# Kernel tuning notes

Measured on AMD Instinct MI355X. Metric: run time of the kernel, lower is better.

Reference implementation:

```python
import jax, jax.numpy as jnp
import numpy as np
from jax import lax

B, L, C_IN, D, H = 256, 4096, 2, 128, 4
DH = D // H          # 32 head dim
FF = 192             # round_up(1.3 * 128, 64)
NUM_CLASSES = 5
EPS = 1e-5


def setup_inputs() -> dict:
    key = jax.random.key(0)
    it = iter(jax.random.split(key, 48))
    def r(*s):
        return jax.random.normal(next(it), s, jnp.float32) * 0.1
    return dict(
        x=jax.random.normal(next(it), (B, L, C_IN), jnp.float32),
        w1a=r(16, C_IN, 4), w1b=r(16, C_IN, 2),
        bn1_g=jnp.ones((32,), jnp.float32), bn1_b=jnp.zeros((32,), jnp.float32),
        bn1_m=r(32), bn1_v=jnp.ones((32,), jnp.float32),
        w2=r(64, 32, 3),
        bn2_g=jnp.ones((64,), jnp.float32), bn2_b=jnp.zeros((64,), jnp.float32),
        bn2_m=r(64), bn2_v=jnp.ones((64,), jnp.float32),
        w3=r(D, 64, 3),
        bn3_g=jnp.ones((D,), jnp.float32), bn3_b=jnp.zeros((D,), jnp.float32),
        bn3_m=r(D), bn3_v=jnp.ones((D,), jnp.float32),
        ln1_w=jnp.ones((D,), jnp.float32),
        conv_w=r(D, 1, 3), conv_b=jnp.zeros((D,), jnp.float32),
        wi=r(H, DH, DH), wf=r(H, DH, DH), wz=r(H, DH, DH), wo=r(H, DH, DH),
        rkernel=r(H, DH, 4, DH), rbias=r(4, H, DH),
        gn_w=jnp.ones((D,), jnp.float32),
        ln2_w=jnp.ones((D,), jnp.float32),
        ffn_up_w=r(D, 2 * FF), ffn_down_w=r(FF, D),
        lnp_w=jnp.ones((D,), jnp.float32),
        fc_w=r(D, NUM_CLASSES), fc_b=jnp.zeros((NUM_CLASSES,), jnp.float32),
        lengths=jnp.full((B,), L, jnp.int32),
    )


def _leaky(x):
    return jnp.where(x >= 0, x, 0.01 * x)


def _bn(x, g, b, m, v):  # eval-mode batchnorm, x: (B, C, L)
    return (x - m[:, None]) * (g / jnp.sqrt(v + EPS))[:, None] + b[:, None]


def _conv(x, w, pad, groups=1):  # x: (B, C, L), w: (O, I/groups, K)
    return lax.conv_general_dilated(x, w, (1,), [pad],
                                    dimension_numbers=('NCH', 'OIH', 'NCH'),
                                    feature_group_count=groups)


def _pool(x):  # max pool kernel=2 stride=2 (floor)
    b, c, l = x.shape
    l2 = l // 2
    return x[:, :, :l2 * 2].reshape(b, c, l2, 2).max(-1)


def _ln(x, w):  # LayerNorm, weight only (xlstm lib default bias=False)
    mu = jnp.mean(x, -1, keepdims=True)
    var = jnp.mean((x - mu) ** 2, -1, keepdims=True)
    return (x - mu) * lax.rsqrt(var + EPS) * w


def _forward(x, w1a, w1b, bn1_g, bn1_b, bn1_m, bn1_v, w2, bn2_g, bn2_b, bn2_m, bn2_v,
             w3, bn3_g, bn3_b, bn3_m, bn3_v, ln1_w, conv_w, conv_b, wi, wf, wz, wo,
             rkernel, rbias, gn_w, ln2_w, ffn_up_w, ffn_down_w, lnp_w, fc_w, fc_b, lengths):
    b = x.shape[0]
    # ---- CNN stem (dropout = identity in eval) ----
    xc = jnp.transpose(x, (0, 2, 1))                      # (B, C_in, L)
    h = jnp.concatenate([_conv(xc, w1a, (1, 1)), _conv(xc, w1b, (0, 0))], 1)  # (B, 32, L-1)
    h = _pool(_leaky(_bn(h, bn1_g, bn1_b, bn1_m, bn1_v)))
    h = _pool(_leaky(_bn(_conv(h, w2, (0, 0)), bn2_g, bn2_b, bn2_m, bn2_v)))
    h = _pool(_leaky(_bn(_conv(h, w3, (0, 0)), bn3_g, bn3_b, bn3_m, bn3_v)))
    e = jnp.transpose(h, (0, 2, 1))                       # (B, S, D)
    s = e.shape[1]

    # ---- sLSTM block: pre-LN -> sLSTM layer -> residual ----
    xn = _ln(e, ln1_w)
    # causal depthwise conv (k=3, left pad 2) + SiLU, feeds i/f gates
    xcv = _conv(jnp.transpose(xn, (0, 2, 1)), conv_w, (2, 0), groups=D)
    xcv = jnp.transpose(jax.nn.silu(xcv + conv_b[:, None]), (0, 2, 1))  # (B, S, D)

    def hproj(t, w):  # headwise (block-diagonal) linear
        return jnp.einsum('bshd,hde->bshe', t.reshape(b, s, H, DH), w)

    gx = jnp.stack([hproj(xcv, wi), hproj(xcv, wf), hproj(xn, wz), hproj(xn, wo)], 2)
    gx = jnp.transpose(gx, (1, 0, 2, 3, 4)) + rbias       # (S, B, 4, H, DH)

    def step(carry, g):
        y, c, n, m = carry                                # each (B, H, DH)
        raw = g + jnp.einsum('bhd,hdge->bghe', y, rkernel)  # (B, 4, H, DH)
        iraw, fraw, zraw, oraw = raw[:, 0], raw[:, 1], raw[:, 2], raw[:, 3]
        logfplusm = m + jax.nn.log_sigmoid(fraw)
        mnew = jnp.maximum(iraw, logfplusm)               # stabilizer
        ig = jnp.exp(iraw - mnew)
        fg = jnp.exp(logfplusm - mnew)
        cnew = fg * c + ig * jnp.tanh(zraw)
        nnew = fg * n + ig
        ynew = jax.nn.sigmoid(oraw) * cnew / nnew
        return (ynew, cnew, nnew, mnew), ynew

    z0 = jnp.zeros((b, H, DH), e.dtype)
    _, ys = lax.scan(step, (z0, z0, z0, z0), gx)          # ys: (S, B, H, DH)
    y = jnp.transpose(ys, (1, 0, 2, 3))                   # (B, S, H, DH)
    mu = jnp.mean(y, -1, keepdims=True)
    var = jnp.mean((y - mu) ** 2, -1, keepdims=True)
    y = ((y - mu) * lax.rsqrt(var + EPS)).reshape(b, s, D) * gn_w  # per-head groupnorm
    e = e + y

    # ---- gated GELU feedforward -> residual ----
    xn2 = _ln(e, ln2_w)
    up = xn2 @ ffn_up_w                                   # (B, S, 2*FF)
    e = e + (jax.nn.gelu(up[..., :FF], approximate=False) * up[..., FF:]) @ ffn_down_w

    # ---- post-stack norm, last token, classifier head ----
    e = _ln(e, lnp_w)
    return e[:, -1, :] @ fc_w + fc_b                      # (B, NUM_CLASSES)


def reference(x, w1a, w1b, bn1_g, bn1_b, bn1_m, bn1_v, w2, bn2_g, bn2_b, bn2_m, bn2_v,
              w3, bn3_g, bn3_b, bn3_m, bn3_v, ln1_w, conv_w, conv_b, wi, wf, wz, wo,
              rkernel, rbias, gn_w, ln2_w, ffn_up_w, ffn_down_w, lnp_w, fc_w, fc_b, lengths):
    return _forward(x, w1a, w1b, bn1_g, bn1_b, bn1_m, bn1_v, w2, bn2_g, bn2_b, bn2_m, bn2_v,
                    w3, bn3_g, bn3_b, bn3_m, bn3_v, ln1_w, conv_w, conv_b, wi, wf, wz, wo,
                    rkernel, rbias, gn_w, ln2_w, ffn_up_w, ffn_down_w, lnp_w, fc_w, fc_b, lengths)
```

## Files before the change

kernel.cpp:

```cpp
#include <hip/hip_runtime.h>
#include <hip/hip_bf16.h>
#include <math.h>

#define EPS 1e-5f

typedef __attribute__((ext_vector_type(8))) _Float16 half8;
typedef __attribute__((ext_vector_type(4))) float f32x4;

static __device__ __forceinline__ unsigned short f16u(float x) {
  _Float16 h = (_Float16)x;
  return *(unsigned short*)&h;
}
static __device__ __forceinline__ float uf16(unsigned short u) {
  _Float16 h = *(_Float16*)&u;
  return (float)h;
}

__global__ __launch_bounds__(256) void kWTB2(const float* __restrict__ w2,
    const float* __restrict__ w3, unsigned short* __restrict__ o2,
    unsigned short* __restrict__ o3) {
  int idx = blockIdx.x * 256 + threadIdx.x;
  if (idx < 64 * 104) {
    int oc = idx / 104, kp = idx % 104;
    float v = 0.f;
    if (kp < 96) { int k = kp >> 5, ci = kp & 31; v = w2[oc * 96 + ci * 3 + k]; }
    o2[idx] = f16u(v);
  } else {
    int j = idx - 64 * 104;
    if (j < 128 * 200) {
      int oc = j / 200, kp = j % 200;
      float v = 0.f;
      if (kp < 192) { int k = kp >> 6, ci = kp & 63; v = w3[oc * 192 + ci * 3 + k]; }
      o3[j] = f16u(v);
    }
  }
}

__global__ __launch_bounds__(512) void kConv12(const float* __restrict__ x,
    const float* __restrict__ w1a, const float* __restrict__ w1b,
    const float* __restrict__ g1, const float* __restrict__ b1,
    const float* __restrict__ m1, const float* __restrict__ v1,
    const unsigned short* __restrict__ Bw, const float* __restrict__ g2,
    const float* __restrict__ b2, const float* __restrict__ m2,
    const float* __restrict__ v2, unsigned short* __restrict__ out2) {
  __shared__ _Float16 sA[130 * 40];
  __shared__ _Float16 sB[64 * 104];
  int tid = threadIdx.x;
  int b = blockIdx.z;
  int p0 = blockIdx.x * 128;
  {
    const unsigned int* src = (const unsigned int*)Bw;
    unsigned int* dst = (unsigned int*)sB;
    for (int i = tid; i < 64 * 104 / 2; i += 512) dst[i] = src[i];
  }
  {
    int c = tid & 31, rg = tid >> 5;
    float sc1 = g1[c] * rsqrtf(v1[c] + EPS);
    float sh1 = b1[c] - m1[c] * sc1;
    float wk0[4], wk1[4];
    if (c < 16) {
#pragma unroll
      for (int k = 0; k < 4; k++) { wk0[k] = w1a[c * 8 + k]; wk1[k] = w1a[c * 8 + 4 + k]; }
    } else {
      int cc = c - 16;
#pragma unroll
      for (int k = 0; k < 2; k++) { wk0[k] = w1b[cc * 4 + k]; wk1[k] = w1b[cc * 4 + 2 + k]; }
      wk0[2] = wk0[3] = wk1[2] = wk1[3] = 0.f;
    }
    const float2* xp = (const float2*)(x + (size_t)b * 8192);
    for (int r = rg; r < 130; r += 16) {
      int rr = p0 + r;
      _Float16 outv = (_Float16)0.f;
      if (rr < 2047) {
        float xv0[5], xv1[5];
#pragma unroll
        for (int j = 0; j < 5; j++) {
          int l = 2 * rr - 1 + j;
          if (l >= 0 && l < 4096) { float2 v = xp[l]; xv0[j] = v.x; xv1[j] = v.y; }
          else { xv0[j] = 0.f; xv1[j] = 0.f; }
        }
        float a0 = 0.f, a1 = 0.f;
        if (c < 16) {
#pragma unroll
          for (int k = 0; k < 4; k++) {
            a0 += xv0[k] * wk0[k] + xv1[k] * wk1[k];
            a1 += xv0[k + 1] * wk0[k] + xv1[k + 1] * wk1[k];
          }
        } else {
#pragma unroll
          for (int k = 0; k < 2; k++) {
            a0 += xv0[k + 1] * wk0[k] + xv1[k + 1] * wk1[k];
            a1 += xv0[k + 2] * wk0[k] + xv1[k + 2] * wk1[k];
          }
        }
        a0 = a0 * sc1 + sh1; a1 = a1 * sc1 + sh1;
        a0 = a0 >= 0.f ? a0 : 0.01f * a0;
        a1 = a1 >= 0.f ? a1 : 0.01f * a1;
        outv = (_Float16)fmaxf(a0, a1);
      }
      sA[r * 40 + c] = outv;
    }
  }
  __syncthreads();
  int lane = tid & 63, w = tid >> 6;
  int nrow = lane & 15, quad = lane >> 4;
  f32x4 acc[4];
#pragma unroll
  for (int i = 0; i < 4; i++) acc[i] = (f32x4){0.f, 0.f, 0.f, 0.f};
  int mbase = w * 16;
#pragma unroll
  for (int kk = 0; kk < 3; kk++) {
    half8 a = *(const half8*)(sA + (mbase + nrow + kk) * 40 + quad * 8);
#pragma unroll
    for (int ot = 0; ot < 4; ot++) {
      half8 bb = *(const half8*)(sB + (ot * 16 + nrow) * 104 + kk * 32 + quad * 8);
      acc[ot] = __builtin_amdgcn_mfma_f32_16x16x32_f16(a, bb, acc[ot], 0, 0, 0);
    }
  }
  int gm0 = p0 + mbase + quad * 4;
#pragma unroll
  for (int ot = 0; ot < 4; ot++) {
    int oc = ot * 16 + nrow;
    float sc = g2[oc] * rsqrtf(v2[oc] + EPS);
    float sh = b2[oc] - m2[oc] * sc;
    float v0 = acc[ot][0] * sc + sh, vv1 = acc[ot][1] * sc + sh;
    float v2e = acc[ot][2] * sc + sh, v3 = acc[ot][3] * sc + sh;
    v0 = v0 >= 0.f ? v0 : 0.01f * v0;
    vv1 = vv1 >= 0.f ? vv1 : 0.01f * vv1;
    v2e = v2e >= 0.f ? v2e : 0.01f * v2e;
    v3 = v3 >= 0.f ? v3 : 0.01f * v3;
    float pA = fmaxf(v0, vv1), pB = fmaxf(v2e, v3);
    int t0 = gm0 >> 1, t1 = t0 + 1;
    if (t0 < 1022) out2[((size_t)b * 1022 + t0) * 64 + oc] = f16u(pA);
    if (t1 < 1022) out2[((size_t)b * 1022 + t1) * 64 + oc] = f16u(pB);
  }
}

__global__ __launch_bounds__(512) void kConv3LN(const unsigned short* __restrict__ in,
    const unsigned short* __restrict__ Bw, const float* __restrict__ g,
    const float* __restrict__ bta, const float* __restrict__ mn,
    const float* __restrict__ vr, const float* __restrict__ lnw,
    unsigned short* __restrict__ xn, float* __restrict__ elast) {
  constexpr int IC = 64, OC = 128, LIN = 1022, AP = 72, BP = 200, KSTEPS = 6, OCT = 8;
  __shared__ _Float16 sA[130 * AP];
  __shared__ _Float16 sB[OC * BP];
  int tid = threadIdx.x;
  int b = blockIdx.z;
  int p0 = blockIdx.x * 128;
  {
    const unsigned int* src = (const unsigned int*)Bw;
    unsigned int* dst = (unsigned int*)sB;
    for (int i = tid; i < OC * BP / 2; i += 512) dst[i] = src[i];
  }
  {
    int q = tid % 8;
    for (int r = tid / 8; r < 130; r += 64) {
      int gp = p0 + r;
      uint4 val = {0u, 0u, 0u, 0u};
      if (gp < LIN) val = *(const uint4*)(in + ((size_t)b * LIN + gp) * IC + q * 8);
      *(uint4*)(sA + r * AP + q * 8) = val;
    }
  }
  __syncthreads();
  int lane = tid & 63, w = tid >> 6;
  int nrow = lane & 15, quad = lane >> 4;
  f32x4 acc[OCT];
#pragma unroll
  for (int i = 0; i < OCT; i++) acc[i] = (f32x4){0.f, 0.f, 0.f, 0.f};
  int mbase = w * 16;
#pragma unroll
  for (int kk = 0; kk < KSTEPS; kk++) {
    int k = kk >> 1;
    int ci0 = (kk & 1) * 32;
    half8 a = *(const half8*)(sA + (mbase + nrow + k) * AP + ci0 + quad * 8);
#pragma unroll
    for (int ot = 0; ot < OCT; ot++) {
      half8 bb = *(const half8*)(sB + (ot * 16 + nrow) * BP + kk * 32 + quad * 8);
      acc[ot] = __builtin_amdgcn_mfma_f32_16x16x32_f16(a, bb, acc[ot], 0, 0, 0);
    }
  }
  float pA[OCT], pB[OCT];
  float sA1 = 0.f, sA2 = 0.f, sB1 = 0.f, sB2 = 0.f;
#pragma unroll
  for (int ot = 0; ot < OCT; ot++) {
    int oc = ot * 16 + nrow;
    float sc = g[oc] * rsqrtf(vr[oc] + EPS);
    float sh = bta[oc] - mn[oc] * sc;
    float v0 = acc[ot][0] * sc + sh, v1 = acc[ot][1] * sc + sh;
    float v2 = acc[ot][2] * sc + sh, v3 = acc[ot][3] * sc + sh;
    v0 = v0 >= 0.f ? v0 : 0.01f * v0;
    v1 = v1 >= 0.f ? v1 : 0.01f * v1;
    v2 = v2 >= 0.f ? v2 : 0.01f * v2;
    v3 = v3 >= 0.f ? v3 : 0.01f * v3;
    float a = fmaxf(v0, v1), bb2 = fmaxf(v2, v3);
    pA[ot] = a; pB[ot] = bb2;
    sA1 += a; sA2 += a * a; sB1 += bb2; sB2 += bb2 * bb2;
  }
#pragma unroll
  for (int m = 1; m <= 8; m <<= 1) {
    sA1 += __shfl_xor(sA1, m); sA2 += __shfl_xor(sA2, m);
    sB1 += __shfl_xor(sB1, m); sB2 += __shfl_xor(sB2, m);
  }
  float muA = sA1 * (1.f / 128.f);
  float rsA = rsqrtf(sA2 * (1.f / 128.f) - muA * muA + EPS);
  float muB = sB1 * (1.f / 128.f);
  float rsB = rsqrtf(sB2 * (1.f / 128.f) - muB * muB + EPS);
  int t0 = (p0 + mbase + quad * 4) >> 1, t1 = t0 + 1;
#pragma unroll
  for (int ot = 0; ot < OCT; ot++) {
    int oc = ot * 16 + nrow;
    float lw = lnw[oc];
    if (t0 < 510) xn[((size_t)b * 510 + t0) * OC + oc] = f16u((pA[ot] - muA) * rsA * lw);
    if (t1 < 510) xn[((size_t)b * 510 + t1) * OC + oc] = f16u((pB[ot] - muB) * rsB * lw);
    if (t1 == 509) elast[b * 128 + oc] = pB[ot];
  }
}

__global__ __launch_bounds__(256) void kGxM(const unsigned short* __restrict__ xn,
    const float* __restrict__ cw, const float* __restrict__ cb,
    const float* __restrict__ wi, const float* __restrict__ wf,
    const float* __restrict__ wz, const float* __restrict__ wo,
    const float* __restrict__ rb, unsigned int* __restrict__ gx) {
  __shared__ __align__(16) char smem[29200];
  float* xnf = (float*)smem;
  _Float16* aX = (_Float16*)(smem + 8720);
  _Float16* aN = (_Float16*)(smem + 13840);
  unsigned short* ct = (unsigned short*)smem;
  _Float16* sW = (_Float16*)(smem + 18960);
  int bh = blockIdx.x, b = bh >> 2, h = bh & 3;
  int tid = threadIdx.x, lane = tid & 63, w = tid >> 6;
  int nrow = lane & 15, quad = lane >> 4;
  for (int idx = tid; idx < 4096; idx += 256) {
    int slot = idx >> 11, n = (idx >> 5) & 63, d = idx & 31;
    const float* wp = slot ? ((n >= 32) ? wo : wz) : ((n >= 32) ? wf : wi);
    sW[slot * 2560 + n * 40 + d] = (_Float16)wp[h * 1024 + d * 32 + (n & 31)];
  }
  int dd = tid & 31;
  float cw0 = cw[(h * 32 + dd) * 3], cw1 = cw[(h * 32 + dd) * 3 + 1],
        cw2 = cw[(h * 32 + dd) * 3 + 2], cbv = cb[h * 32 + dd];
  float bias0[4], bias1[4];
#pragma unroll
  for (int nt = 0; nt < 4; nt++) {
    int n = nt * 16 + nrow;
    bias0[nt] = rb[(n >> 5) * 128 + h * 32 + (n & 31)];
    bias1[nt] = rb[(2 + (n >> 5)) * 128 + h * 32 + (n & 31)];
  }
  __syncthreads();
  half8 bw0[4], bw1[4];
#pragma unroll
  for (int nt = 0; nt < 4; nt++) {
    bw0[nt] = *(const half8*)(sW + (nt * 16 + nrow) * 40 + quad * 8);
    bw1[nt] = *(const half8*)(sW + 2560 + (nt * 16 + nrow) * 40 + quad * 8);
  }
  const unsigned short* xb = xn + ((size_t)b * 510) * 128 + h * 32;
  for (int s0 = 0; s0 < 510; s0 += 64) {
    __syncthreads();
    {
      int d2 = tid & 15;
      for (int r = tid >> 4; r < 66; r += 16) {
        int s = s0 - 2 + r;
        unsigned int v = 0;
        if (s >= 0 && s < 510) v = *(const unsigned int*)(xb + (size_t)s * 128 + d2 * 2);
        xnf[r * 33 + d2 * 2]     = uf16(v & 0xFFFFu);
        xnf[r * 33 + d2 * 2 + 1] = uf16(v >> 16);
      }
    }
    __syncthreads();
    for (int m = tid >> 5; m < 64; m += 8) {
      float x0 = xnf[m * 33 + dd], x1 = xnf[(m + 1) * 33 + dd], x2 = xnf[(m + 2) * 33 + dd];
      float a = cbv + cw0 * x0 + cw1 * x1 + cw2 * x2;
      a = a * __builtin_amdgcn_rcpf(1.f + __expf(-a));
      aX[m * 40 + dd] = (_Float16)a;
      aN[m * 40 + dd] = (_Float16)x2;
    }
    __syncthreads();
    f32x4 z = (f32x4){0.f, 0.f, 0.f, 0.f};
    half8 ax = *(const half8*)(aX + (w * 16 + nrow) * 40 + quad * 8);
    half8 an = *(const half8*)(aN + (w * 16 + nrow) * 40 + quad * 8);
    f32x4 acc0[4], acc1[4];
#pragma unroll
    for (int nt = 0; nt < 4; nt++) {
      acc0[nt] = __builtin_amdgcn_mfma_f32_16x16x32_f16(ax, bw0[nt], z, 0, 0, 0);
      acc1[nt] = __builtin_amdgcn_mfma_f32_16x16x32_f16(an, bw1[nt], z, 0, 0, 0);
    }
    __syncthreads();
#pragma unroll
    for (int nt = 0; nt < 4; nt++) {
#pragma unroll
      for (int r = 0; r < 4; r++) {
        int row = w * 16 + quad * 4 + r;
        ct[row * 132 + 2 * (nt * 16 + nrow)]     = f16u(acc0[nt][r] + bias0[nt]);
        ct[row * 132 + 2 * (nt * 16 + nrow) + 1] = f16u(acc1[nt][r] + bias1[nt]);
      }
    }
    __syncthreads();
    {
      int u = tid & 63;
      for (int m = tid >> 6; m < 64; m += 4) {
        int s = s0 + m;
        if (s < 510)
          gx[((size_t)s * 1024 + bh) * 64 + u] = *(const unsigned int*)(ct + m * 132 + 2 * u);
      }
    }
  }
}

__global__ __launch_bounds__(64) void kRec(const unsigned int* __restrict__ gx,
    const float* __restrict__ rk, float* __restrict__ yf) {
  int bh = blockIdx.x; int h = bh & 3;
  int l = threadIdx.x; int half = l >> 5; int e = l & 31;
  float R1[32], R2[32];
  int g1 = half, g2 = 2 + half;
  const float* r1p = rk + h * 4096 + g1 * 32 + e;
  const float* r2p = rk + h * 4096 + g2 * 32 + e;
#pragma unroll
  for (int d = 0; d < 32; d++) { R1[d] = r1p[d * 128]; R2[d] = r2p[d * 128]; }
  const unsigned int* gp = gx + (size_t)bh * 64 + l;
  unsigned int p0 = gp[0], p1 = gp[65536], p2 = gp[131072], p3 = gp[196608];
  float y = 0.f, cst = 0.f, nst = 0.f, mst = 0.f;
  for (int s = 0; s < 510; s++) {
    unsigned int pc = p0; p0 = p1; p1 = p2; p2 = p3;
    if (s + 4 < 510) p3 = gp[(size_t)(s + 4) * 65536];
    float a1 = uf16(pc & 0xFFFFu);
    float a2 = uf16(pc >> 16);
    float s10 = 0.f, s11 = 0.f, s12 = 0.f, s13 = 0.f;
    float s20 = 0.f, s21 = 0.f, s22 = 0.f, s23 = 0.f;
    unsigned int yb = __float_as_uint(y);
#pragma unroll
    for (int d = 0; d < 32; d += 4) {
      float y0 = __uint_as_float(__builtin_amdgcn_readlane(yb, d));
      float y1 = __uint_as_float(__builtin_amdgcn_readlane(yb, d + 1));
      float y2 = __uint_as_float(__builtin_amdgcn_readlane(yb, d + 2));
      float y3 = __uint_as_float(__builtin_amdgcn_readlane(yb, d + 3));
      s10 = fmaf(y0, R1[d], s10);     s20 = fmaf(y0, R2[d], s20);
      s11 = fmaf(y1, R1[d + 1], s11); s21 = fmaf(y1, R2[d + 1], s21);
      s12 = fmaf(y2, R1[d + 2], s12); s22 = fmaf(y2, R2[d + 2], s22);
      s13 = fmaf(y3, R1[d + 3], s13); s23 = fmaf(y3, R2[d + 3], s23);
    }
    a1 += (s10 + s11) + (s12 + s13);
    a2 += (s20 + s21) + (s22 + s23);
    float en = __expf(-fabsf(a1));
    float ls = fminf(a1, 0.f) - __logf(1.f + en);
    float sg = __builtin_amdgcn_rcpf(1.f + __expf(-a2));
    float tz = 1.f - 2.f * __builtin_amdgcn_rcpf(__expf(2.f * a2) + 1.f);
    float lsf = __shfl_xor(ls, 32);
    float so  = __shfl_xor(sg, 32);
    float lf = mst + lsf;
    float mnew = fmaxf(a1, lf);
    float ig = __expf(a1 - mnew);
    float fg = __expf(lf - mnew);
    cst = fg * cst + ig * tz;
    nst = fg * nst + ig;
    mst = mnew;
    y = so * cst * __builtin_amdgcn_rcpf(nst);
  }
  if (half == 0) yf[(bh >> 2) * 128 + h * 32 + e] = y;
}

__global__ __launch_bounds__(128) void kHead(const float* __restrict__ yf,
    const float* __restrict__ elast, const float* __restrict__ gnw,
    const float* __restrict__ ln2w, const float* __restrict__ upw,
    const float* __restrict__ dnw, const float* __restrict__ lnpw,
    const float* __restrict__ fcw, const float* __restrict__ fcb,
    float* __restrict__ outp) {
  int c = threadIdx.x; int b = blockIdx.x;
  __shared__ float sred[4];
  __shared__ float sx[128];
  __shared__ float sup[384];
  __shared__ float shh[192];
  float yv = yf[b * 128 + c];
  float s1 = yv, s2 = yv * yv;
#pragma unroll
  for (int m = 1; m <= 16; m <<= 1) { s1 += __shfl_xor(s1, m); s2 += __shfl_xor(s2, m); }
  float mu = s1 * (1.f / 32.f);
  float var = s2 * (1.f / 32.f) - mu * mu;
  float yn = (yv - mu) * rsqrtf(var + EPS) * gnw[c];
  float el = elast[b * 128 + c] + yn;
  auto ln128 = [&](float v, const float* w) -> float {
    float a = v, a2 = v * v;
#pragma unroll
    for (int m = 1; m <= 32; m <<= 1) { a += __shfl_xor(a, m); a2 += __shfl_xor(a2, m); }
    int wv = c >> 6;
    if ((c & 63) == 0) { sred[wv * 2] = a; sred[wv * 2 + 1] = a2; }
    __syncthreads();
    float t1 = sred[0] + sred[2], t2 = sred[1] + sred[3];
    __syncthreads();
    float mm = t1 * (1.f / 128.f);
    float vv = t2 * (1.f / 128.f) - mm * mm;
    return (v - mm) * rsqrtf(vv + EPS) * w[c];
  };
  float xn2 = ln128(el, ln2w);
  sx[c] = xn2;
  __syncthreads();
#pragma unroll
  for (int jj = 0; jj < 3; jj++) {
    int j = c + jj * 128;
    float acc = 0.f;
    for (int k = 0; k < 128; k++) acc += sx[k] * upw[k * 384 + j];
    sup[j] = acc;
  }
  __syncthreads();
  {
    float u = sup[c]; float mg = sup[192 + c];
    shh[c] = 0.5f * u * (1.f + erff(u * 0.70710678118654752f)) * mg;
    if (c < 64) {
      float u2 = sup[128 + c]; float m2 = sup[320 + c];
      shh[128 + c] = 0.5f * u2 * (1.f + erff(u2 * 0.70710678118654752f)) * m2;
    }
  }
  __syncthreads();
  float acc = 0.f;
  for (int f = 0; f < 192; f++) acc += shh[f] * dnw[f * 128 + c];
  float e2 = el + acc;
  float e3 = ln128(e2, lnpw);
  sx[c] = e3;
  __syncthreads();
  if (c < 5) {
    float a = fcb[c];
    for (int k = 0; k < 128; k++) a += sx[k] * fcw[k * 5 + c];
    outp[b * 5 + c] = a;
  }
}

extern "C" void kernel_launch(void* const* d_in, const int* in_sizes, int n_in,
                              void* d_out, int out_size, void* d_ws, size_t ws_size,
                              hipStream_t stream) {
  const float* x    = (const float*)d_in[0];
  const float* w1a  = (const float*)d_in[1];
  const float* w1b  = (const float*)d_in[2];
  const float* bn1g = (const float*)d_in[3];
  const float* bn1b = (const float*)d_in[4];
  const float* bn1m = (const float*)d_in[5];
  const float* bn1v = (const float*)d_in[6];
  const float* w2   = (const float*)d_in[7];
  const float* bn2g = (const float*)d_in[8];
  const float* bn2b = (const float*)d_in[9];
  const float* bn2m = (const float*)d_in[10];
  const float* bn2v = (const float*)d_in[11];
  const float* w3   = (const float*)d_in[12];
  const float* bn3g = (const float*)d_in[13];
  const float* bn3b = (const float*)d_in[14];
  const float* bn3m = (const float*)d_in[15];
  const float* bn3v = (const float*)d_in[16];
  const float* ln1w = (const float*)d_in[17];
  const float* cw   = (const float*)d_in[18];
  const float* cb   = (const float*)d_in[19];
  const float* wi   = (const float*)d_in[20];
  const float* wf   = (const float*)d_in[21];
  const float* wz   = (const float*)d_in[22];
  const float* wo   = (const float*)d_in[23];
  const float* rk   = (const float*)d_in[24];
  const float* rb   = (const float*)d_in[25];
  const float* gnw  = (const float*)d_in[26];
  const float* ln2w = (const float*)d_in[27];
  const float* upw  = (const float*)d_in[28];
  const float* dnw  = (const float*)d_in[29];
  const float* lnpw = (const float*)d_in[30];
  const float* fcw  = (const float*)d_in[31];
  const float* fcb  = (const float*)d_in[32];
  float* outp = (float*)d_out;

  char* ws = (char*)d_ws;
  unsigned short* xnb  = (unsigned short*)ws;
  unsigned short* out2 = (unsigned short*)(ws + ((size_t)64 << 20));
  unsigned int*   gxu  = (unsigned int*)(ws + ((size_t)128 << 20));
  float* elast = (float*)(ws + ((size_t)258 << 20));
  float* yfin  = (float*)(ws + ((size_t)259 << 20));
  unsigned short* wtg2 = (unsigned short*)(ws + ((size_t)260 << 20));
  unsigned short* wtg3 = (unsigned short*)(ws + ((size_t)260 << 20) + (1 << 20));

  kWTB2<<<dim3(126), 256, 0, stream>>>(w2, w3, wtg2, wtg3);
  kConv12<<<dim3(16, 1, 256), 512, 0, stream>>>(
      x, w1a, w1b, bn1g, bn1b, bn1m, bn1v, wtg2, bn2g, bn2b, bn2m, bn2v, out2);
  kConv3LN<<<dim3(8, 1, 256), 512, 0, stream>>>(
      out2, wtg3, bn3g, bn3b, bn3m, bn3v, ln1w, xnb, elast);
  kGxM<<<dim3(1024), 256, 0, stream>>>(xnb, cw, cb, wi, wf, wz, wo, rb, gxu);
  kRec<<<dim3(1024), 64, 0, stream>>>(gxu, rk, yfin);
  kHead<<<dim3(256), 128, 0, stream>>>(yfin, elast, gnw, ln2w, upw, dnw, lnpw, fcw, fcb, outp);
}
```

Before: 608.8 us.

## Use fp16 dot2 recurrence via LDS and fold weight conversion into conv kernels

The recurrent kernel now stores the hidden state in shared memory as fp16 and computes the recurrent matvec with packed fp16 dot2 instructions, replacing the readlane broadcasts and scalar FMAs. Recurrent weights are held as packed halves, which halves their register footprint. The sigmoid and tanh are merged into a single exp/rcp per lane. Separately, the weight-transpose pre-kernel is removed and each conv block converts the fp32 weights into LDS itself, saving one launch at the cost of redundant per-block conversion. This risks accuracy loss from fp16 state and weights over 510 serial steps, and the per-step LDS write then read has no explicit barrier, relying on the 64-thread block being a single wavefront.

```diff
diff --git a/kernel.cpp b/kernel.cpp
--- a/kernel.cpp
+++ b/kernel.cpp
@@ -5,6 +5,7 @@
 #define EPS 1e-5f
 
 typedef __attribute__((ext_vector_type(8))) _Float16 half8;
+typedef __attribute__((ext_vector_type(2))) _Float16 half2v;
 typedef __attribute__((ext_vector_type(4))) float f32x4;
 
 static __device__ __forceinline__ unsigned short f16u(float x) {
@@ -15,32 +16,19 @@
   _Float16 h = *(_Float16*)&u;
   return (float)h;
 }
-
-__global__ __launch_bounds__(256) void kWTB2(const float* __restrict__ w2,
-    const float* __restrict__ w3, unsigned short* __restrict__ o2,
-    unsigned short* __restrict__ o3) {
-  int idx = blockIdx.x * 256 + threadIdx.x;
-  if (idx < 64 * 104) {
-    int oc = idx / 104, kp = idx % 104;
-    float v = 0.f;
-    if (kp < 96) { int k = kp >> 5, ci = kp & 31; v = w2[oc * 96 + ci * 3 + k]; }
-    o2[idx] = f16u(v);
-  } else {
-    int j = idx - 64 * 104;
-    if (j < 128 * 200) {
-      int oc = j / 200, kp = j % 200;
-      float v = 0.f;
-      if (kp < 192) { int k = kp >> 6, ci = kp & 63; v = w3[oc * 192 + ci * 3 + k]; }
-      o3[j] = f16u(v);
-    }
-  }
+static __device__ __forceinline__ float fdot2f(half2v a, half2v b, float c) {
+#if __has_builtin(__builtin_amdgcn_fdot2)
+  return __builtin_amdgcn_fdot2(a, b, c, false);
+#else
+  return c + (float)a[0] * (float)b[0] + (float)a[1] * (float)b[1];
+#endif
 }
 
 __global__ __launch_bounds__(512) void kConv12(const float* __restrict__ x,
     const float* __restrict__ w1a, const float* __restrict__ w1b,
     const float* __restrict__ g1, const float* __restrict__ b1,
     const float* __restrict__ m1, const float* __restrict__ v1,
-    const unsigned short* __restrict__ Bw, const float* __restrict__ g2,
+    const float* __restrict__ w2, const float* __restrict__ g2,
     const float* __restrict__ b2, const float* __restrict__ m2,
     const float* __restrict__ v2, unsigned short* __restrict__ out2) {
   __shared__ _Float16 sA[130 * 40];
@@ -48,10 +36,11 @@
   int tid = threadIdx.x;
   int b = blockIdx.z;
   int p0 = blockIdx.x * 128;
-  {
-    const unsigned int* src = (const unsigned int*)Bw;
-    unsigned int* dst = (unsigned int*)sB;
-    for (int i = tid; i < 64 * 104 / 2; i += 512) dst[i] = src[i];
+  for (int i = tid; i < 64 * 104; i += 512) {
+    int oc = i / 104, kp = i - oc * 104;
+    float v = 0.f;
+    if (kp < 96) v = w2[oc * 96 + (kp & 31) * 3 + (kp >> 5)];
+    sB[i] = (_Float16)v;
   }
   {
     int c = tid & 31, rg = tid >> 5;
@@ -137,7 +126,7 @@
 }
 
 __global__ __launch_bounds__(512) void kConv3LN(const unsigned short* __restrict__ in,
-    const unsigned short* __restrict__ Bw, const float* __restrict__ g,
+    const float* __restrict__ w3, const float* __restrict__ g,
     const float* __restrict__ bta, const float* __restrict__ mn,
     const float* __restrict__ vr, const float* __restrict__ lnw,
     unsigned short* __restrict__ xn, float* __restrict__ elast) {
@@ -147,10 +136,11 @@
   int tid = threadIdx.x;
   int b = blockIdx.z;
   int p0 = blockIdx.x * 128;
-  {
-    const unsigned int* src = (const unsigned int*)Bw;
-    unsigned int* dst = (unsigned int*)sB;
-    for (int i = tid; i < OC * BP / 2; i += 512) dst[i] = src[i];
+  for (int i = tid; i < 128 * 200; i += 512) {
+    int oc = i / 200, kp = i - oc * 200;
+    float v = 0.f;
+    if (kp < 192) v = w3[oc * 192 + (kp & 63) * 3 + (kp >> 6)];
+    sB[i] = (_Float16)v;
   }
   {
     int q = tid % 8;
@@ -307,44 +297,51 @@
 
 __global__ __launch_bounds__(64) void kRec(const unsigned int* __restrict__ gx,
     const float* __restrict__ rk, float* __restrict__ yf) {
+  __shared__ _Float16 ybuf[64];
   int bh = blockIdx.x; int h = bh & 3;
   int l = threadIdx.x; int half = l >> 5; int e = l & 31;
-  float R1[32], R2[32];
+  half2v R1p[16], R2p[16];
   int g1 = half, g2 = 2 + half;
   const float* r1p = rk + h * 4096 + g1 * 32 + e;
   const float* r2p = rk + h * 4096 + g2 * 32 + e;
 #pragma unroll
-  for (int d = 0; d < 32; d++) { R1[d] = r1p[d * 128]; R2[d] = r2p[d * 128]; }
+  for (int d = 0; d < 16; d++) {
+    R1p[d] = (half2v){(_Float16)r1p[(2 * d) * 128], (_Float16)r1p[(2 * d + 1) * 128]};
+    R2p[d] = (half2v){(_Float16)r2p[(2 * d) * 128], (_Float16)r2p[(2 * d + 1) * 128]};
+  }
   const unsigned int* gp = gx + (size_t)bh * 64 + l;
   unsigned int p0 = gp[0], p1 = gp[65536], p2 = gp[131072], p3 = gp[196608];
   float y = 0.f, cst = 0.f, nst = 0.f, mst = 0.f;
+  ybuf[l] = (_Float16)0.f;
   for (int s = 0; s < 510; s++) {
     unsigned int pc = p0; p0 = p1; p1 = p2; p2 = p3;
     if (s + 4 < 510) p3 = gp[(size_t)(s + 4) * 65536];
     float a1 = uf16(pc & 0xFFFFu);
     float a2 = uf16(pc >> 16);
-    float s10 = 0.f, s11 = 0.f, s12 = 0.f, s13 = 0.f;
-    float s20 = 0.f, s21 = 0.f, s22 = 0.f, s23 = 0.f;
-    unsigned int yb = __float_as_uint(y);
-#pragma unroll
-    for (int d = 0; d < 32; d += 4) {
-      float y0 = __uint_as_float(__builtin_amdgcn_readlane(yb, d));
-      float y1 = __uint_as_float(__builtin_amdgcn_readlane(yb, d + 1));
-      float y2 = __uint_as_float(__builtin_amdgcn_readlane(yb, d + 2));
-      float y3 = __uint_as_float(__builtin_amdgcn_readlane(yb, d + 3));
-      s10 = fmaf(y0, R1[d], s10);     s20 = fmaf(y0, R2[d], s20);
-      s11 = fmaf(y1, R1[d + 1], s11); s21 = fmaf(y1, R2[d + 1], s21);
-      s12 = fmaf(y2, R1[d + 2], s12); s22 = fmaf(y2, R2[d + 2], s22);
-      s13 = fmaf(y3, R1[d + 3], s13); s23 = fmaf(y3, R2[d + 3], s23);
-    }
-    a1 += (s10 + s11) + (s12 + s13);
-    a2 += (s20 + s21) + (s22 + s23);
+    _Float16 yl[32];
+    *(half8*)(yl)      = *(const half8*)(ybuf);
+    *(half8*)(yl + 8)  = *(const half8*)(ybuf + 8);
+    *(half8*)(yl + 16) = *(const half8*)(ybuf + 16);
+    *(half8*)(yl + 24) = *(const half8*)(ybuf + 24);
+    float s1a = 0.f, s1b = 0.f, s2a = 0.f, s2b = 0.f;
+#pragma unroll
+    for (int d = 0; d < 16; d += 2) {
+      half2v ya = *(const half2v*)(yl + 2 * d);
+      half2v yb = *(const half2v*)(yl + 2 * d + 2);
+      s1a = fdot2f(ya, R1p[d], s1a);
+      s1b = fdot2f(yb, R1p[d + 1], s1b);
+      s2a = fdot2f(ya, R2p[d], s2a);
+      s2b = fdot2f(yb, R2p[d + 1], s2b);
+    }
+    a1 += s1a + s1b;
+    a2 += s2a + s2b;
     float en = __expf(-fabsf(a1));
     float ls = fminf(a1, 0.f) - __logf(1.f + en);
-    float sg = __builtin_amdgcn_rcpf(1.f + __expf(-a2));
-    float tz = 1.f - 2.f * __builtin_amdgcn_rcpf(__expf(2.f * a2) + 1.f);
+    float u = half ? a2 : (a2 + a2);
+    float su = __builtin_amdgcn_rcpf(1.f + __expf(-u));
+    float tz = su + su - 1.f;
     float lsf = __shfl_xor(ls, 32);
-    float so  = __shfl_xor(sg, 32);
+    float so  = __shfl_xor(su, 32);
     float lf = mst + lsf;
     float mnew = fmaxf(a1, lf);
     float ig = __expf(a1 - mnew);
@@ -353,6 +350,7 @@
     nst = fg * nst + ig;
     mst = mnew;
     y = so * cst * __builtin_amdgcn_rcpf(nst);
+    ybuf[l] = (_Float16)y;
   }
   if (half == 0) yf[(bh >> 2) * 128 + h * 32 + e] = y;
 }
@@ -466,14 +464,11 @@
   unsigned int*   gxu  = (unsigned int*)(ws + ((size_t)128 << 20));
   float* elast = (float*)(ws + ((size_t)258 << 20));
   float* yfin  = (float*)(ws + ((size_t)259 << 20));
-  unsigned short* wtg2 = (unsigned short*)(ws + ((size_t)260 << 20));
-  unsigned short* wtg3 = (unsigned short*)(ws + ((size_t)260 << 20) + (1 << 20));
-
-  kWTB2<<<dim3(126), 256, 0, stream>>>(w2, w3, wtg2, wtg3);
+
   kConv12<<<dim3(16, 1, 256), 512, 0, stream>>>(
-      x, w1a, w1b, bn1g, bn1b, bn1m, bn1v, wtg2, bn2g, bn2b, bn2m, bn2v, out2);
+      x, w1a, w1b, bn1g, bn1b, bn1m, bn1v, w2, bn2g, bn2b, bn2m, bn2v, out2);
   kConv3LN<<<dim3(8, 1, 256), 512, 0, stream>>>(
-      out2, wtg3, bn3g, bn3b, bn3m, bn3v, ln1w, xnb, elast);
+      out2, w3, bn3g, bn3b, bn3m, bn3v, ln1w, xnb, elast);
   kGxM<<<dim3(1024), 256, 0, stream>>>(xnb, cw, cb, wi, wf, wz, wo, rb, gxu);
   kRec<<<dim3(1024), 64, 0, stream>>>(gxu, rk, yfin);
   kHead<<<dim3(256), 128, 0, stream>>>(yfin, elast, gnw, ln2w, upw, dnw, lnpw, fcw, fcb, outp);
```

Measured after the change: 645.9 us. +6.1%, slower.
